# Optimization experiments

Hardware: AMD Instinct MI355X
Metric: run time of the kernel (lower is better)

The kernel has to match this reference:

```python
import jax, jax.numpy as jnp
import numpy as np

NUM_NODES = 100000
NUM_EDGES = 640000
D_IN = 128
D_OUT = 128


def setup_inputs() -> dict:
    key = jax.random.key(0)
    k_x, k_s, k_t, k_w, k_lin = jax.random.split(key, 5)
    x = jax.random.normal(k_x, (NUM_NODES, D_IN), dtype=jnp.float32)
    source = jax.random.randint(k_s, (NUM_EDGES,), 0, NUM_NODES, dtype=jnp.int32)
    target = jax.random.randint(k_t, (NUM_EDGES,), 0, NUM_NODES, dtype=jnp.int32)
    edge_weights = jax.random.uniform(k_w, (NUM_EDGES,), dtype=jnp.float32)
    # nn.Linear weight, shape (out, in), kaiming-uniform-ish init
    bound = 1.0 / np.sqrt(D_IN)
    W = jax.random.uniform(k_lin, (D_OUT, D_IN), dtype=jnp.float32, minval=-bound, maxval=bound)
    return {"x": x, "W": W, "edge_weights": edge_weights, "source": source, "target": target}


def reference(x, W, edge_weights, source, target):
    # LinearMessageCreator: project all nodes first (as in the torch code), then gather per edge
    h = jnp.einsum("nd,od->no", x, W)            # (num_nodes, d_out)
    msg = h[source] * edge_weights[:, None]       # (num_edges, d_out)
    # SumAggregator: scatter-add messages into target nodes
    delta = jax.ops.segment_sum(msg, target, num_segments=x.shape[0])
    # OnlyUpdate: return aggregated messages
    return delta
```

## Files before the change

### kernel.cpp

```cpp
#include <hip/hip_runtime.h>
#include <hip/hip_bf16.h>

#define NN 100000
#define NE 640000
#define D 128

#define SCAN_CHUNK 1024
#define NBLK ((NN + SCAN_CHUNK - 1) / SCAN_CHUNK)

#define OFF_COUNTS  0u
#define OFF_OFFSETS 400000u
#define OFF_CURSOR  800016u
#define OFF_BSUM    1200016u
#define OFF_BSUMEX  1200528u
#define OFF_PE      1201040u
#define WS_T2       6321040u
#define OFF_XB      6321040u
#define WS_FULL     31921040u

__device__ __forceinline__ float bflo(unsigned u) { return __uint_as_float(u << 16); }
__device__ __forceinline__ float bfhi(unsigned u) { return __uint_as_float(u & 0xffff0000u); }

__global__ __launch_bounds__(256) void k_hist(const int* __restrict__ tgt,
                                              int* __restrict__ counts) {
    int e = blockIdx.x * 256 + threadIdx.x;
    if (e < NE) atomicAdd(&counts[tgt[e]], 1);
}

__global__ __launch_bounds__(256) void k_scan_part(const int* __restrict__ counts,
                                                   int* __restrict__ bsum) {
    __shared__ int sd[256];
    int b = blockIdx.x, t = threadIdx.x;
    int base = b * SCAN_CHUNK + t * 4;
    int s = 0;
    #pragma unroll
    for (int k = 0; k < 4; ++k) { int i = base + k; s += (i < NN) ? counts[i] : 0; }
    sd[t] = s; __syncthreads();
    for (int off = 128; off > 0; off >>= 1) {
        if (t < off) sd[t] += sd[t + off];
        __syncthreads();
    }
    if (t == 0) bsum[b] = sd[0];
}

__global__ __launch_bounds__(128) void k_scan_mid(const int* __restrict__ bsum,
                                                  int* __restrict__ bsumex,
                                                  int* __restrict__ offsets) {
    __shared__ int sd[128];
    int t = threadIdx.x;
    int v = (t < NBLK) ? bsum[t] : 0;
    sd[t] = v; __syncthreads();
    for (int off = 1; off < 128; off <<= 1) {
        int tmp = (t >= off) ? sd[t - off] : 0;
        __syncthreads();
        sd[t] += tmp;
        __syncthreads();
    }
    if (t < NBLK) bsumex[t] = sd[t] - v;
    if (t == 0) offsets[NN] = NE;
}

__global__ __launch_bounds__(256) void k_scan_final(const int* __restrict__ counts,
                                                    const int* __restrict__ bsumex,
                                                    int* __restrict__ offsets,
                                                    int* __restrict__ cursor) {
    __shared__ int sd[256];
    int b = blockIdx.x, t = threadIdx.x;
    int base = b * SCAN_CHUNK + t * 4;
    int c[4]; int s = 0;
    #pragma unroll
    for (int k = 0; k < 4; ++k) { int i = base + k; c[k] = (i < NN) ? counts[i] : 0; s += c[k]; }
    sd[t] = s; __syncthreads();
    for (int off = 1; off < 256; off <<= 1) {
        int tmp = (t >= off) ? sd[t - off] : 0;
        __syncthreads();
        sd[t] += tmp;
        __syncthreads();
    }
    int run = sd[t] - s + bsumex[b];
    #pragma unroll
    for (int k = 0; k < 4; ++k) {
        int i = base + k;
        if (i < NN) { offsets[i] = run; cursor[i] = run; }
        run += c[k];
    }
}

__global__ __launch_bounds__(256) void k_fill(const int* __restrict__ src,
                                              const int* __restrict__ tgt,
                                              const float* __restrict__ ew,
                                              int* __restrict__ cursor,
                                              int2* __restrict__ pe) {
    int e = blockIdx.x * 256 + threadIdx.x;
    if (e < NE) {
        int t = tgt[e];
        int p = atomicAdd(&cursor[t], 1);
        pe[p] = make_int2(src[e], __float_as_int(ew[e]));
    }
}

__global__ __launch_bounds__(256) void k_conv(const float* __restrict__ x,
                                              unsigned* __restrict__ xb) {
    int i = blockIdx.x * 256 + threadIdx.x;
    if (i < NN * 64) {
        float2 v = ((const float2*)x)[i];
        __hip_bfloat16 b0 = __float2bfloat16(v.x);
        __hip_bfloat16 b1 = __float2bfloat16(v.y);
        unsigned u0 = *(const unsigned short*)&b0;
        unsigned u1 = *(const unsigned short*)&b1;
        xb[i] = u0 | (u1 << 16);
    }
}

__global__ __launch_bounds__(256) void k_gather_bf(const unsigned* __restrict__ xb,
                                                   const int* __restrict__ offsets,
                                                   const int2* __restrict__ pe,
                                                   float* __restrict__ out) {
    int wid = blockIdx.x * 4 + (threadIdx.x >> 6);
    int lane = threadIdx.x & 63;
    if (wid >= NN) return;
    int beg = offsets[wid], end = offsets[wid + 1];
    float a0 = 0.f, a1 = 0.f;
    int2 e = (beg < end) ? pe[beg] : make_int2(0, 0);
    for (int i = beg; i < end; ++i) {
        int2 en = (i + 1 < end) ? pe[i + 1] : make_int2(0, 0);
        unsigned v = xb[(size_t)e.x * 64 + lane];
        float w = __int_as_float(e.y);
        a0 = fmaf(bflo(v), w, a0);
        a1 = fmaf(bfhi(v), w, a1);
        e = en;
    }
    ((float2*)out)[(size_t)wid * 64 + lane] = make_float2(a0, a1);
}

__global__ __launch_bounds__(256) void k_gather_f32(const float* __restrict__ x,
                                                    const int* __restrict__ offsets,
                                                    const int2* __restrict__ pe,
                                                    float* __restrict__ out) {
    int wid = blockIdx.x * 4 + (threadIdx.x >> 6);
    int lane = threadIdx.x & 63;
    if (wid >= NN) return;
    int beg = offsets[wid], end = offsets[wid + 1];
    const float2* x2 = (const float2*)x;
    float a0 = 0.f, a1 = 0.f;
    int2 e = (beg < end) ? pe[beg] : make_int2(0, 0);
    for (int i = beg; i < end; ++i) {
        int2 en = (i + 1 < end) ? pe[i + 1] : make_int2(0, 0);
        float2 v = x2[(size_t)e.x * 64 + lane];
        float w = __int_as_float(e.y);
        a0 = fmaf(v.x, w, a0);
        a1 = fmaf(v.y, w, a1);
        e = en;
    }
    ((float2*)out)[(size_t)wid * 64 + lane] = make_float2(a0, a1);
}

#define PBN 64

__global__ __launch_bounds__(256) void k_project(const float* __restrict__ W,
                                                 float* __restrict__ io) {
    __shared__ __align__(16) float xs[PBN][D];
    __shared__ __align__(16) __hip_bfloat16 Wb[D][D];

    const int tid = threadIdx.x;

    const float4* W4 = (const float4*)W;
    for (int k = 0; k < 16; ++k) {
        int idx = k * 256 + tid;
        int f = idx & 127;
        int dq = idx >> 7;
        float4 v = W4[(size_t)f * 32 + dq];
        Wb[dq * 4 + 0][f] = __float2bfloat16(v.x);
        Wb[dq * 4 + 1][f] = __float2bfloat16(v.y);
        Wb[dq * 4 + 2][f] = __float2bfloat16(v.z);
        Wb[dq * 4 + 3][f] = __float2bfloat16(v.w);
    }

    const long nb = (long)blockIdx.x * PBN;
    const float4* io4 = (const float4*)io;
    for (int k = 0; k < 8; ++k) {
        int idx = k * 256 + tid;
        int n = idx >> 5;
        int dq = idx & 31;
        long node = nb + n;
        float4 v = (node < NN) ? io4[node * 32 + dq] : make_float4(0.f, 0.f, 0.f, 0.f);
        *(float4*)&xs[n][dq * 4] = v;
    }
    __syncthreads();

    const int fg = tid & 15;
    const int ng = tid >> 4;
    float acc[4][8];
    #pragma unroll
    for (int r = 0; r < 4; ++r)
        #pragma unroll
        for (int ff = 0; ff < 8; ++ff) acc[r][ff] = 0.f;

    for (int d = 0; d < D; d += 4) {
        float4 xv[4];
        #pragma unroll
        for (int r = 0; r < 4; ++r) xv[r] = *(const float4*)&xs[ng * 4 + r][d];
        #pragma unroll
        for (int j = 0; j < 4; ++j) {
            uint4 wv = *(const uint4*)&Wb[d + j][fg * 8];
            float wf0 = bflo(wv.x), wf1 = bfhi(wv.x);
            float wf2 = bflo(wv.y), wf3 = bfhi(wv.y);
            float wf4 = bflo(wv.z), wf5 = bfhi(wv.z);
            float wf6 = bflo(wv.w), wf7 = bfhi(wv.w);
            #pragma unroll
            for (int r = 0; r < 4; ++r) {
                float xj = ((const float*)&xv[r])[j];
                acc[r][0] = fmaf(xj, wf0, acc[r][0]);
                acc[r][1] = fmaf(xj, wf1, acc[r][1]);
                acc[r][2] = fmaf(xj, wf2, acc[r][2]);
                acc[r][3] = fmaf(xj, wf3, acc[r][3]);
                acc[r][4] = fmaf(xj, wf4, acc[r][4]);
                acc[r][5] = fmaf(xj, wf5, acc[r][5]);
                acc[r][6] = fmaf(xj, wf6, acc[r][6]);
                acc[r][7] = fmaf(xj, wf7, acc[r][7]);
            }
        }
    }

    #pragma unroll
    for (int r = 0; r < 4; ++r) {
        long node = nb + ng * 4 + r;
        if (node < NN) {
            float4* dst = (float4*)&io[node * D + fg * 8];
            dst[0] = make_float4(acc[r][0], acc[r][1], acc[r][2], acc[r][3]);
            dst[1] = make_float4(acc[r][4], acc[r][5], acc[r][6], acc[r][7]);
        }
    }
}

__global__ __launch_bounds__(256) void gcn_scatter(const float* __restrict__ x,
                                                   const float* __restrict__ ew,
                                                   const int* __restrict__ src,
                                                   const int* __restrict__ tgt,
                                                   float* __restrict__ out) {
    int tid = blockIdx.x * 256 + threadIdx.x;
    int e = tid >> 5;
    int t = tid & 31;
    if (e >= NE) return;
    int s = src[e];
    int g = tgt[e];
    float w = ew[e];
    float4 xv = reinterpret_cast<const float4*>(x)[s * 32 + t];
    float* dst = out + (size_t)g * D + (t << 2);
    atomicAdd(dst + 0, xv.x * w);
    atomicAdd(dst + 1, xv.y * w);
    atomicAdd(dst + 2, xv.z * w);
    atomicAdd(dst + 3, xv.w * w);
}

extern "C" void kernel_launch(void* const* d_in, const int* in_sizes, int n_in,
                              void* d_out, int out_size, void* d_ws, size_t ws_size,
                              hipStream_t stream) {
    const float* x   = (const float*)d_in[0];
    const float* W   = (const float*)d_in[1];
    const float* ew  = (const float*)d_in[2];
    const int*   src = (const int*)d_in[3];
    const int*   tgt = (const int*)d_in[4];
    float* out = (float*)d_out;

    if (ws_size >= WS_T2) {
        char* ws = (char*)d_ws;
        int*  counts  = (int*)(ws + OFF_COUNTS);
        int*  offsets = (int*)(ws + OFF_OFFSETS);
        int*  cursor  = (int*)(ws + OFF_CURSOR);
        int*  bsum    = (int*)(ws + OFF_BSUM);
        int*  bsumex  = (int*)(ws + OFF_BSUMEX);
        int2* pe      = (int2*)(ws + OFF_PE);

        hipMemsetAsync(counts, 0, (size_t)NN * sizeof(int), stream);
        k_hist<<<(NE + 255) / 256, 256, 0, stream>>>(tgt, counts);
        k_scan_part<<<NBLK, 256, 0, stream>>>(counts, bsum);
        k_scan_mid<<<1, 128, 0, stream>>>(bsum, bsumex, offsets);
        k_scan_final<<<NBLK, 256, 0, stream>>>(counts, bsumex, offsets, cursor);
        k_fill<<<(NE + 255) / 256, 256, 0, stream>>>(src, tgt, ew, cursor, pe);

        if (ws_size >= WS_FULL) {
            unsigned* xb = (unsigned*)(ws + OFF_XB);
            k_conv<<<(NN * 64 + 255) / 256, 256, 0, stream>>>(x, xb);
            k_gather_bf<<<(NN + 3) / 4, 256, 0, stream>>>(xb, offsets, pe, out);
        } else {
            k_gather_f32<<<(NN + 3) / 4, 256, 0, stream>>>(x, offsets, pe, out);
        }
    } else {
        hipMemsetAsync(out, 0, (size_t)out_size * sizeof(float), stream);
        gcn_scatter<<<(NE * 32 + 255) / 256, 256, 0, stream>>>(x, ew, src, tgt, out);
    }

    k_project<<<(NN + PBN - 1) / PBN, 256, 0, stream>>>(W, out);
}
```

Baseline: 294.1 us.

## Replace scalar-FMA projection kernel with bf16 MFMA matrix-core GEMM

```diff
diff --git a/kernel.cpp b/kernel.cpp
--- a/kernel.cpp
+++ b/kernel.cpp
@@ -18,8 +18,15 @@
 #define OFF_XB      6321040u
 #define WS_FULL     31921040u
 
+typedef __attribute__((ext_vector_type(8))) short bf16x8;
+typedef __attribute__((ext_vector_type(4))) float f32x4;
+
 __device__ __forceinline__ float bflo(unsigned u) { return __uint_as_float(u << 16); }
 __device__ __forceinline__ float bfhi(unsigned u) { return __uint_as_float(u & 0xffff0000u); }
+__device__ __forceinline__ unsigned bfpk(float x, float y) {
+    __hip_bfloat16 bx = __float2bfloat16(x), by = __float2bfloat16(y);
+    return (unsigned)(*(unsigned short*)&bx) | ((unsigned)(*(unsigned short*)&by) << 16);
+}
 
 __global__ __launch_bounds__(256) void k_hist(const int* __restrict__ tgt,
                                               int* __restrict__ counts) {
@@ -104,11 +111,7 @@
     int i = blockIdx.x * 256 + threadIdx.x;
     if (i < NN * 64) {
         float2 v = ((const float2*)x)[i];
-        __hip_bfloat16 b0 = __float2bfloat16(v.x);
-        __hip_bfloat16 b1 = __float2bfloat16(v.y);
-        unsigned u0 = *(const unsigned short*)&b0;
-        unsigned u1 = *(const unsigned short*)&b1;
-        xb[i] = u0 | (u1 << 16);
+        xb[i] = bfpk(v.x, v.y);
     }
 }
 
@@ -155,80 +158,59 @@
     ((float2*)out)[(size_t)wid * 64 + lane] = make_float2(a0, a1);
 }
 
-#define PBN 64
-
-__global__ __launch_bounds__(256) void k_project(const float* __restrict__ W,
-                                                 float* __restrict__ io) {
-    __shared__ __align__(16) float xs[PBN][D];
-    __shared__ __align__(16) __hip_bfloat16 Wb[D][D];
+#define KP 136
+
+__global__ __launch_bounds__(256) void k_project_mfma(const float* __restrict__ W,
+                                                      float* __restrict__ io) {
+    __shared__ unsigned short Wb[D][KP];
+    __shared__ unsigned short As[64][KP];
 
     const int tid = threadIdx.x;
+    const long nb = (long)blockIdx.x * 64;
 
     const float4* W4 = (const float4*)W;
-    for (int k = 0; k < 16; ++k) {
-        int idx = k * 256 + tid;
-        int f = idx & 127;
-        int dq = idx >> 7;
-        float4 v = W4[(size_t)f * 32 + dq];
-        Wb[dq * 4 + 0][f] = __float2bfloat16(v.x);
-        Wb[dq * 4 + 1][f] = __float2bfloat16(v.y);
-        Wb[dq * 4 + 2][f] = __float2bfloat16(v.z);
-        Wb[dq * 4 + 3][f] = __float2bfloat16(v.w);
-    }
-
-    const long nb = (long)blockIdx.x * PBN;
+    #pragma unroll
+    for (int it = 0; it < 16; ++it) {
+        int idx = it * 256 + tid;
+        int f = idx >> 5, kq = idx & 31;
+        float4 v = W4[idx];
+        *(uint2*)&Wb[f][kq * 4] = make_uint2(bfpk(v.x, v.y), bfpk(v.z, v.w));
+    }
     const float4* io4 = (const float4*)io;
-    for (int k = 0; k < 8; ++k) {
-        int idx = k * 256 + tid;
-        int n = idx >> 5;
-        int dq = idx & 31;
+    #pragma unroll
+    for (int it = 0; it < 8; ++it) {
+        int idx = it * 256 + tid;
+        int n = idx >> 5, kq = idx & 31;
         long node = nb + n;
-        float4 v = (node < NN) ? io4[node * 32 + dq] : make_float4(0.f, 0.f, 0.f, 0.f);
-        *(float4*)&xs[n][dq * 4] = v;
+        float4 v = (node < NN) ? io4[node * 32 + kq]
+                               : make_float4(0.f, 0.f, 0.f, 0.f);
+        *(uint2*)&As[n][kq * 4] = make_uint2(bfpk(v.x, v.y), bfpk(v.z, v.w));
     }
     __syncthreads();
 
-    const int fg = tid & 15;
-    const int ng = tid >> 4;
-    float acc[4][8];
-    #pragma unroll
-    for (int r = 0; r < 4; ++r)
+    const int w  = tid >> 6;
+    const int l  = tid & 63;
+    const int lr = l & 15;
+    const int lg = l >> 4;
+    const int r0 = w * 16;
+
+    bf16x8 afrag[4];
+    #pragma unroll
+    for (int ks = 0; ks < 4; ++ks)
+        afrag[ks] = *(const bf16x8*)&As[r0 + lr][ks * 32 + lg * 8];
+
+    #pragma unroll
+    for (int ct = 0; ct < 8; ++ct) {
+        f32x4 acc = {0.f, 0.f, 0.f, 0.f};
         #pragma unroll
-        for (int ff = 0; ff < 8; ++ff) acc[r][ff] = 0.f;
-
-    for (int d = 0; d < D; d += 4) {
-        float4 xv[4];
+        for (int ks = 0; ks < 4; ++ks) {
+            bf16x8 bfrag = *(const bf16x8*)&Wb[ct * 16 + lr][ks * 32 + lg * 8];
+            acc = __builtin_amdgcn_mfma_f32_16x16x32_bf16(afrag[ks], bfrag, acc, 0, 0, 0);
+        }
         #pragma unroll
-        for (int r = 0; r < 4; ++r) xv[r] = *(const float4*)&xs[ng * 4 + r][d];
-        #pragma unroll
-        for (int j = 0; j < 4; ++j) {
-            uint4 wv = *(const uint4*)&Wb[d + j][fg * 8];
-            float wf0 = bflo(wv.x), wf1 = bfhi(wv.x);
-            float wf2 = bflo(wv.y), wf3 = bfhi(wv.y);
-            float wf4 = bflo(wv.z), wf5 = bfhi(wv.z);
-            float wf6 = bflo(wv.w), wf7 = bfhi(wv.w);
-            #pragma unroll
-            for (int r = 0; r < 4; ++r) {
-                float xj = ((const float*)&xv[r])[j];
-                acc[r][0] = fmaf(xj, wf0, acc[r][0]);
-                acc[r][1] = fmaf(xj, wf1, acc[r][1]);
-                acc[r][2] = fmaf(xj, wf2, acc[r][2]);
-                acc[r][3] = fmaf(xj, wf3, acc[r][3]);
-                acc[r][4] = fmaf(xj, wf4, acc[r][4]);
-                acc[r][5] = fmaf(xj, wf5, acc[r][5]);
-                acc[r][6] = fmaf(xj, wf6, acc[r][6]);
-                acc[r][7] = fmaf(xj, wf7, acc[r][7]);
-            }
-        }
-    }
-
-    #pragma unroll
-    for (int r = 0; r < 4; ++r) {
-        long node = nb + ng * 4 + r;
-        if (node < NN) {
-            float4* dst = (float4*)&io[node * D + fg * 8];
-            dst[0] = make_float4(acc[r][0], acc[r][1], acc[r][2], acc[r][3]);
-            dst[1] = make_float4(acc[r][4], acc[r][5], acc[r][6], acc[r][7]);
+        for (int r = 0; r < 4; ++r) {
+            long gn = nb + r0 + lg * 4 + r;
+            if (gn < NN) io[gn * D + ct * 16 + lr] = acc[r];
         }
     }
 }
@@ -291,5 +273,5 @@
         gcn_scatter<<<(NE * 32 + 255) / 256, 256, 0, stream>>>(x, ew, src, tgt, out);
     }
 
-    k_project<<<(NN + PBN - 1) / PBN, 256, 0, stream>>>(W, out);
-}
+    k_project_mfma<<<(NN + 63) / 64, 256, 0, stream>>>(W, out);
+}
```

Result: faster. 261.1 us (-11.2%).
